# Kernel optimization log

Measured on AMD Instinct MI355X. Metric: run time of the kernel, lower is better.

The kernel has to match this reference:

```python
import jax, jax.numpy as jnp
import numpy as np

B, D_IN, D_HID, D_OUT = 16384, 512, 512, 512
E, K = 8, 2
VQ_COEFF, LB_COEFF = 0.05, 0.01
LOG100 = float(np.log(100.0))
LOG2 = float(np.log(2.0))


def _normalize(v):
    # torch F.normalize(dim=1): x / max(||x||, 1e-12)
    n = jnp.linalg.norm(v, axis=-1, keepdims=True)
    return v / jnp.maximum(n, 1e-12)


def _cv_squared(v):
    # torch .var() is unbiased (ddof=1)
    return jnp.var(v, ddof=1) / (jnp.mean(v) ** 2 + 1e-10)


def _rbm_layer(x, rm, W, b, ca, temp):
    # x: [B, d_in], rm: [E, d_in], W: [E, d_out, d_in], b: [E, d_out]
    rm_n = jax.lax.stop_gradient(_normalize(rm))          # .detach() in source
    nx = _normalize(x)
    dists = nx @ rm_n.T                                    # [B, E]
    top_v, top_i = jax.lax.top_k(dists, K)                 # [B, K]
    tv = jax.nn.softmax(top_v, axis=-1)                    # softmax over top-k
    bsz = dists.shape[0]
    attn = jnp.zeros_like(dists).at[jnp.arange(bsz)[:, None], top_i].set(tv)
    # const_attention is frozen (requires_grad=False)
    inp_att = jnp.exp(jnp.minimum(jax.lax.stop_gradient(ca), LOG100))  # [E]
    # dense gather-compute-scatter: expert e output for every token, masked by attn
    eo = jnp.einsum('bi,eoi->beo', x, W) * inp_att[None, :, None] + b[None, :, :]
    out = jnp.einsum('be,beo->bo', jax.lax.stop_gradient(attn), eo)    # att.detach()
    out = out * jnp.exp(jnp.minimum(temp, LOG100))
    # aux losses (eval mode: no EMA memory update)
    vq = -(nx[:, None, :] * rm_n[top_i]).sum(-1)           # [B, K]
    vq_loss = (tv * vq).sum(-1).mean()
    lb = _cv_squared(attn.sum(0))
    aux = VQ_COEFF * vq_loss + LB_COEFF * lb               # sim_coeff = 0
    return out, aux


def setup_inputs() -> dict:
    key = jax.random.key(0)
    ks = jax.random.split(key, 8)
    x = jax.random.normal(ks[0], (B, D_IN), dtype=jnp.float32)
    rm0 = _normalize(jax.random.normal(ks[1], (E, D_IN), dtype=jnp.float32))
    W0 = jax.random.normal(ks[2], (E, D_HID, D_IN), dtype=jnp.float32) / np.sqrt(D_IN)
    b0 = jnp.zeros((E, D_HID), dtype=jnp.float32)
    rm1 = _normalize(jax.random.normal(ks[3], (E, D_HID), dtype=jnp.float32))
    W1 = jax.random.normal(ks[4], (E, D_OUT, D_HID), dtype=jnp.float32) / np.sqrt(D_HID)
    b1 = jnp.zeros((E, D_OUT), dtype=jnp.float32)
    temp0 = jnp.full((1,), LOG2, dtype=jnp.float32)
    temp1 = jnp.full((1,), LOG2, dtype=jnp.float32)
    ca0 = jnp.zeros((E,), dtype=jnp.float32)
    ca1 = jnp.zeros((E,), dtype=jnp.float32)
    return {"x": x, "rm0": rm0, "W0": W0, "b0": b0, "temp0": temp0, "ca0": ca0,
            "rm1": rm1, "W1": W1, "b1": b1, "temp1": temp1, "ca1": ca1}


def reference(x, rm0, W0, b0, temp0, ca0, rm1, W1, b1, temp1, ca1):
    h0, a0 = _rbm_layer(x, rm0, W0, b0, ca0, temp0)
    h_emb = h0                      # embedding tapped after layer 0 (pre-activation)
    h = jax.nn.relu(h0)             # norm_type=None -> no norm
    h1, a1 = _rbm_layer(h, rm1, W1, b1, ca1, temp1)
    return (h_emb, h1, a0 + a1)
```

## Files before the change

### kernel.cpp

```cpp
#include <hip/hip_runtime.h>
#include <cmath>
#include <cstdint>

#define NTOK   16384
#define NEXP   8
#define DM     512
#define LOG100 4.605170185988092f

typedef _Float16 half8  __attribute__((ext_vector_type(8)));
typedef float    floatx4 __attribute__((ext_vector_type(4)));

#define MFMA_F16(a, b, c) __builtin_amdgcn_mfma_f32_16x16x32_f16((a), (b), (c), 0, 0, 0)

__device__ __forceinline__ void gl_lds16(const void* g, void* l) {
    __builtin_amdgcn_global_load_lds(
        (const __attribute__((address_space(1))) void*)g,
        (__attribute__((address_space(3))) void*)l, 16, 0, 0);
}


__global__ __launch_bounds__(256) void prep_kernel(
    const float* __restrict__ rm0, const float* __restrict__ rm1,
    const float* __restrict__ ca0, const float* __restrict__ ca1,
    const float* __restrict__ temp0, const float* __restrict__ temp1,
    float* __restrict__ ctrl, float* __restrict__ rmn)
{
    int tid = threadIdx.x, lane = tid & 63, w = tid >> 6;
    if (tid < 32) ((int*)ctrl)[tid] = 0;
    if (tid >= 32 && tid < 48) ctrl[tid] = 0.f;
    if (tid == 48 || tid == 49) ctrl[tid] = 0.f;
    if (tid == 50) ctrl[50] = expf(fminf(temp0[0], LOG100));
    if (tid == 51) ctrl[51] = expf(fminf(temp1[0], LOG100));
    if (tid >= 52 && tid < 68) {
        int i = tid - 52;
        ctrl[tid] = expf(fminf(i < 8 ? ca0[i] : ca1[i - 8], LOG100));
    }
    for (int r = w; r < 16; r += 4) {
        const float* src = (r < 8) ? (rm0 + r * DM) : (rm1 + (r - 8) * DM);
        float v[8]; float ss = 0.f;
        #pragma unroll
        for (int j = 0; j < 8; ++j) { v[j] = src[lane + 64 * j]; ss += v[j] * v[j]; }
        #pragma unroll
        for (int off = 32; off > 0; off >>= 1) ss += __shfl_xor(ss, off);
        float inv = 1.f / fmaxf(sqrtf(ss), 1e-12f);
        float* dst = rmn + r * DM;
        #pragma unroll
        for (int j = 0; j < 8; ++j) dst[lane + 64 * j] = v[j] * inv;
    }
}

__global__ __launch_bounds__(256) void pack_w_kernel(
    const float* __restrict__ W0, const float* __restrict__ W1,
    half8* __restrict__ w0pk, half8* __restrict__ w1pk)
{
    int i = blockIdx.x * 256 + threadIdx.x;
    if (i < 512 * 1024) {
        int l = i & 63, j = (i >> 6) & 15, kb = (i >> 10) & 15, nt = (i >> 14) & 3, e = i >> 16;
        int s = l >> 3, p = l & 7, c = p ^ s;
        int n = nt * 128 + j * 8 + s;
        int k = kb * 32 + (c & 3) * 8;
        const float* src = W0 + ((size_t)e * DM + n) * DM + k;
        half8 v;
        #pragma unroll
        for (int t = 0; t < 8; ++t) {
            float f = src[t];
            _Float16 h = (_Float16)f;
            v[t] = (c < 4) ? h : (_Float16)(f - (float)h);
        }
        w0pk[i] = v;
    } else {
        int m = i - 512 * 1024;
        int l = m & 63, j = (m >> 6) & 15, kb = (m >> 10) & 7, nt = (m >> 13) & 3, e = m >> 15;
        int s = l >> 3, p = l & 7, c = p ^ s;
        int n = nt * 128 + j * 8 + s;
        int k = kb * 64 + c * 8;
        const float* src = W1 + ((size_t)e * DM + n) * DM + k;
        half8 v;
        #pragma unroll
        for (int t = 0; t < 8; ++t) v[t] = (_Float16)src[t];
        w1pk[m] = v;
    }
}

__global__ __launch_bounds__(256) void route_kernel(
    const float* __restrict__ src,
    const float* __restrict__ rmn,
    int relu_in, int split,
    _Float16* __restrict__ dst,
    unsigned char* __restrict__ key,
    float2* __restrict__ wts,
    float2* __restrict__ bs)
{
    __shared__ float rmLds[NEXP * DM];
    int tid = threadIdx.x;
    for (int i = tid; i < NEXP * DM; i += 256) rmLds[i] = rmn[i];
    __syncthreads();
    int lane = tid & 63, w = tid >> 6;
    int token = blockIdx.x * 4 + w;

    const float* row = src + (size_t)token * DM;
    float x[8]; float ss = 0.f;
    #pragma unroll
    for (int j = 0; j < 8; ++j) {
        float v = row[lane + 64 * j];
        if (relu_in) v = fmaxf(v, 0.f);
        x[j] = v; ss += v * v;
    }
    if (split) {
        #pragma unroll
        for (int j = 0; j < 8; ++j) {
            int k = lane + 64 * j;
            size_t base = (size_t)token * 1024 + (size_t)((k >> 5) << 6) + (k & 31);
            _Float16 h = (_Float16)x[j];
            dst[base] = h;
            dst[base + 32] = (_Float16)(x[j] - (float)h);
        }
    } else {
        #pragma unroll
        for (int j = 0; j < 8; ++j)
            dst[(size_t)token * DM + lane + 64 * j] = (_Float16)x[j];
    }
    float d[8];
    #pragma unroll
    for (int e = 0; e < 8; ++e) {
        float a = 0.f;
        #pragma unroll
        for (int j = 0; j < 8; ++j) a += x[j] * rmLds[e * DM + lane + 64 * j];
        d[e] = a;
    }
    #pragma unroll
    for (int off = 32; off > 0; off >>= 1) {
        ss += __shfl_xor(ss, off);
        #pragma unroll
        for (int e = 0; e < 8; ++e) d[e] += __shfl_xor(d[e], off);
    }
    float inv = 1.f / fmaxf(sqrtf(ss), 1e-12f);
    float best = -1e30f, second = -1e30f; int be = 0, se = 0;
    #pragma unroll
    for (int e = 0; e < 8; ++e) {
        float de = d[e] * inv;
        if (de > best)        { second = best; se = be; best = de; be = e; }
        else if (de > second) { second = de; se = e; }
    }
    float z = expf(second - best);
    float w0 = 1.f / (1.f + z), w1 = z / (1.f + z);
    if (lane == 0) {
        key[token] = (unsigned char)be;
        key[NTOK + token] = (unsigned char)se;
        wts[token] = make_float2(w0, w1);
        bs[token] = make_float2(best, second);
    }
}

__global__ __launch_bounds__(256) void compact_kernel(
    const unsigned char* __restrict__ key,
    const float2* __restrict__ wts,
    const float2* __restrict__ bs,
    int* __restrict__ cnt,
    unsigned short* __restrict__ bkt,
    float* __restrict__ imp,
    float* __restrict__ vq_acc)
{
    int slot = blockIdx.x >> 3, e = blockIdx.x & 7;
    int chunk = blockIdx.y;
    const unsigned char* k = key + slot * NTOK;
    unsigned short* ob = bkt + (size_t)(slot * 8 + e) * NTOK;
    int tid = threadIdx.x, lane = tid & 63, w = tid >> 6;
    float wsum = 0.f, vqs = 0.f;
    for (int c = 0; c < 8; ++c) {
        int tok = chunk * 2048 + c * 256 + tid;
        bool m = (k[tok] == (unsigned char)e);
        unsigned long long mask = __ballot(m);
        int wcount = __popcll(mask);
        int wbase = 0;
        if (lane == 0 && wcount) wbase = atomicAdd(&cnt[slot * 8 + e], wcount);
        wbase = __shfl(wbase, 0);
        if (m) {
            int pre = __popcll(mask & ((1ull << lane) - 1ull));
            ob[wbase + pre] = (unsigned short)tok;
            float2 wp = wts[tok]; float2 b2 = bs[tok];
            float wv = slot ? wp.y : wp.x;
            wsum += wv;
            vqs  += wv * (slot ? b2.y : b2.x);
        }
    }
    #pragma unroll
    for (int off = 32; off > 0; off >>= 1) {
        wsum += __shfl_xor(wsum, off);
        vqs  += __shfl_xor(vqs, off);
    }
    __shared__ float rw[4], rv[4];
    if (lane == 0) { rw[w] = wsum; rv[w] = vqs; }
    __syncthreads();
    if (tid == 0) {
        atomicAdd(&imp[e], rw[0] + rw[1] + rw[2] + rw[3]);
        atomicAdd(vq_acc, -(rv[0] + rv[1] + rv[2] + rv[3]));
    }
}

template <bool SPLIT>
__global__ __launch_bounds__(256, 3) void gemm_kernel(
    const _Float16* __restrict__ A,
    const _Float16* __restrict__ Wpk,
    const float* __restrict__ bias,
    const float* __restrict__ iav,
    const float* __restrict__ tscp,
    const int* __restrict__ cnt,
    const unsigned short* __restrict__ bkt,
    const float2* __restrict__ wts,
    int slot, int accum,
    float* __restrict__ outp)
{
    __shared__ __align__(16) _Float16 ldsB[2 * 8192];
    __shared__ int tokLds[128];

    int p = blockIdx.x;
    int xcd = p & 7, s = p >> 3;
    int t = xcd * 17 + (s >> 2), nt = s & 3;
    int e = -1, m0 = 0, M = 0, acc0 = 0;
    #pragma unroll
    for (int ee = 0; ee < 8; ++ee) {
        int Me = cnt[ee];
        int ne = (Me + 127) >> 7;
        if (t >= acc0 && t < acc0 + ne) { e = ee; m0 = (t - acc0) << 7; M = Me; }
        acc0 += ne;
    }
    if (e < 0) return;
    int n0 = nt << 7;
    int valid = min(128, M - m0);
    int tid = threadIdx.x, lane = tid & 63, w = tid >> 6;
    if (tid < 128) tokLds[tid] = bkt[e * NTOK + m0 + min(tid, valid - 1)];
    __syncthreads();

    int wm = w >> 1, wn = w & 1;
    int r0 = wm * 64, c0 = wn * 64;
    int q = lane >> 4, l15 = lane & 15;

    constexpr int KIT = SPLIT ? 16 : 8;
    constexpr int AS  = SPLIT ? 1024 : 512;

    const _Float16* Ab[4];
    #pragma unroll
    for (int mi = 0; mi < 4; ++mi)
        Ab[mi] = A + (size_t)tokLds[r0 + mi * 16 + l15] * AS + q * 8;

    const _Float16* wtile = Wpk + (size_t)(e * 4 + nt) * KIT * 8192;

    floatx4 accu[4][4];
    #pragma unroll
    for (int mi = 0; mi < 4; ++mi)
        #pragma unroll
        for (int ni = 0; ni < 4; ++ni) accu[mi][ni] = (floatx4){0.f, 0.f, 0.f, 0.f};

    #pragma unroll
    for (int jj = 0; jj < 4; ++jj) {
        int j = w + jj * 4;
        gl_lds16(wtile + j * 512 + lane * 8, (void*)(ldsB + j * 512));
    }

    #pragma unroll
    for (int kb = 0; kb < KIT; ++kb) {
        half8 ah[4], al[4];
        #pragma unroll
        for (int mi = 0; mi < 4; ++mi) {
            ah[mi] = *(const half8*)(Ab[mi] + kb * 64);
            al[mi] = *(const half8*)(Ab[mi] + kb * 64 + 32);
        }
        if (kb + 1 < KIT) {
            _Float16* dB = ldsB + ((kb + 1) & 1) * 8192;
            const _Float16* wb = wtile + (size_t)(kb + 1) * 8192;
            #pragma unroll
            for (int jj = 0; jj < 4; ++jj) {
                int j = w + jj * 4;
                gl_lds16(wb + j * 512 + lane * 8, (void*)(dB + j * 512));
            }
        }
        if (kb + 1 < KIT) asm volatile("s_waitcnt vmcnt(12)" ::: "memory");
        else              asm volatile("s_waitcnt vmcnt(8)"  ::: "memory");
        __builtin_amdgcn_sched_barrier(0);
        __builtin_amdgcn_s_barrier();
        {
            const _Float16* bB = ldsB + (kb & 1) * 8192;
            #pragma unroll
            for (int ni = 0; ni < 4; ++ni) {
                int r = c0 + ni * 16 + l15;
                int ph = q ^ (r & 7), pl = (q + 4) ^ (r & 7);
                half8 bh = *(const half8*)(bB + r * 64 + ph * 8);
                half8 bl = *(const half8*)(bB + r * 64 + pl * 8);
                if constexpr (SPLIT) {
                    #pragma unroll
                    for (int mi = 0; mi < 4; ++mi) accu[mi][ni] = MFMA_F16(ah[mi], bh, accu[mi][ni]);
                    #pragma unroll
                    for (int mi = 0; mi < 4; ++mi) accu[mi][ni] = MFMA_F16(ah[mi], bl, accu[mi][ni]);
                    #pragma unroll
                    for (int mi = 0; mi < 4; ++mi) accu[mi][ni] = MFMA_F16(al[mi], bh, accu[mi][ni]);
                } else {
                    #pragma unroll
                    for (int mi = 0; mi < 4; ++mi) accu[mi][ni] = MFMA_F16(ah[mi], bh, accu[mi][ni]);
                    #pragma unroll
                    for (int mi = 0; mi < 4; ++mi) accu[mi][ni] = MFMA_F16(al[mi], bl, accu[mi][ni]);
                }
            }
        }
        if (kb + 1 < KIT) {
            __builtin_amdgcn_sched_barrier(0);
            __builtin_amdgcn_s_barrier();
        }
    }

    float tsc = *tscp, iae = iav[e];
    float bv[4];
    #pragma unroll
    for (int ni = 0; ni < 4; ++ni) bv[ni] = bias[e * DM + n0 + c0 + ni * 16 + l15];
    #pragma unroll
    for (int mi = 0; mi < 4; ++mi) {
        int liBase = r0 + mi * 16 + q * 4;
        #pragma unroll
        for (int reg = 0; reg < 4; ++reg) {
            int li = liBase + reg;
            if (li < valid) {
                int tok = tokLds[li];
                float2 wp = wts[tok];
                float wgt = slot ? wp.y : wp.x;
                float sg = tsc * wgt * iae, sb = tsc * wgt;
                float* orow = outp + (size_t)tok * DM + n0;
                #pragma unroll
                for (int ni = 0; ni < 4; ++ni) {
                    float v = accu[mi][ni][reg] * sg + bv[ni] * sb;
                    int c = c0 + ni * 16 + l15;
                    if (accum) orow[c] += v; else orow[c] = v;
                }
            }
        }
    }
}

__global__ void finalize_kernel(const float* __restrict__ ctrl, float* __restrict__ outp)
{
    if (threadIdx.x == 0) {
        float aux = 0.f;
        for (int l = 0; l < 2; ++l) {
            float vq = ctrl[48 + l] / (float)NTOK;
            float mean = 0.f;
            for (int e = 0; e < 8; ++e) mean += ctrl[32 + l * 8 + e];
            mean *= 0.125f;
            float s = 0.f;
            for (int e = 0; e < 8; ++e) {
                float d = ctrl[32 + l * 8 + e] - mean;
                s += d * d;
            }
            float var = s / 7.f;
            float lb = var / (mean * mean + 1e-10f);
            aux += 0.05f * vq + 0.01f * lb;
        }
        *outp = aux;
    }
}

extern "C" void kernel_launch(void* const* d_in, const int* in_sizes, int n_in,
                              void* d_out, int out_size, void* d_ws, size_t ws_size,
                              hipStream_t stream) {
    const float* x     = (const float*)d_in[0];
    const float* rm0   = (const float*)d_in[1];
    const float* W0    = (const float*)d_in[2];
    const float* b0    = (const float*)d_in[3];
    const float* temp0 = (const float*)d_in[4];
    const float* ca0   = (const float*)d_in[5];
    const float* rm1   = (const float*)d_in[6];
    const float* W1    = (const float*)d_in[7];
    const float* b1    = (const float*)d_in[8];
    const float* temp1 = (const float*)d_in[9];
    const float* ca1   = (const float*)d_in[10];
    float* out = (float*)d_out;

    char* ws = (char*)d_ws;
    float* ctrl = (float*)ws;
    int*   cnt  = (int*)ctrl;
    float* imp  = ctrl + 32;
    float* vq   = ctrl + 48;
    float* tsc  = ctrl + 50;
    float* ia   = ctrl + 52;
    float* rmn  = ctrl + 128;
    float2*        wts = (float2*)(ws + (size_t)64  * 1024);
    float2*        bs  = (float2*)(ws + (size_t)384 * 1024);
    unsigned char* key = (unsigned char*)(ws + (size_t)704 * 1024);

    char* big = ws + (1 << 20);
    half8*          w0pk8 = (half8*)(big);
    half8*          w1pk8 = (half8*)(big + (size_t)8  * 1024 * 1024);
    const _Float16* w0pk  = (const _Float16*)w0pk8;
    const _Float16* w1pk  = (const _Float16*)w1pk8;
    _Float16*       h16   = (_Float16*)(big + (size_t)12 * 1024 * 1024);
    unsigned short* bkt   = (unsigned short*)(big + (size_t)28 * 1024 * 1024);

    _Float16* xpk = (_Float16*)(out + (size_t)NTOK * DM);

    prep_kernel<<<1, 256, 0, stream>>>(rm0, rm1, ca0, ca1, temp0, temp1, ctrl, rmn);
    pack_w_kernel<<<3072, 256, 0, stream>>>(W0, W1, w0pk8, w1pk8);

    route_kernel<<<4096, 256, 0, stream>>>(x, rmn, 0, 1, xpk, key, wts, bs);
    compact_kernel<<<dim3(16, 8), 256, 0, stream>>>(key, wts, bs, cnt, bkt, imp, vq);
    gemm_kernel<true><<<544, 256, 0, stream>>>(xpk, w0pk, b0, ia, tsc,
        cnt, bkt, wts, 0, 0, out);
    gemm_kernel<true><<<544, 256, 0, stream>>>(xpk, w0pk, b0, ia, tsc,
        cnt + 8, bkt + 8 * NTOK, wts, 1, 1, out);

    route_kernel<<<4096, 256, 0, stream>>>(out, rmn + 4096, 1, 0, h16,
        key + 2 * NTOK, wts + NTOK, bs + NTOK);
    compact_kernel<<<dim3(16, 8), 256, 0, stream>>>(key + 2 * NTOK, wts + NTOK, bs + NTOK,
        cnt + 16, bkt + 16 * NTOK, imp + 8, vq + 1);
    gemm_kernel<false><<<544, 256, 0, stream>>>(h16, w1pk, b1, ia + 8, tsc + 1,
        cnt + 16, bkt + 16 * NTOK, wts + NTOK, 0, 0, out + (size_t)NTOK * DM);
    gemm_kernel<false><<<544, 256, 0, stream>>>(h16, w1pk, b1, ia + 8, tsc + 1,
        cnt + 24, bkt + 24 * NTOK, wts + NTOK, 1, 1, out + (size_t)NTOK * DM);

    finalize_kernel<<<1, 64, 0, stream>>>(ctrl, out + (size_t)2 * NTOK * DM);
}
```

Baseline: 485.3 us.

## Merge top-k slot GEMMs into one atomic-accumulating launch and fold prep into pack

The two per-slot expert GEMM launches in each layer become one launch over 16 buckets (slot × expert). Both slots now add into the output with fp32 global atomic adds, and the route kernel zeroes each output row beforehand. The separate prep kernel is folded into an extra block of the weight-pack kernel, and GEMM launch bounds rise to 4 waves per SIMD. The aim is fewer launches, less serialization between slot passes and better tail fill, at the cost of atomic traffic, extra zero-store bandwidth, nondeterministic summation order and possible register pressure.

```diff
diff --git a/kernel.cpp b/kernel.cpp
--- a/kernel.cpp
+++ b/kernel.cpp
@@ -18,41 +18,48 @@
         (__attribute__((address_space(3))) void*)l, 16, 0, 0);
 }
 
-
-__global__ __launch_bounds__(256) void prep_kernel(
+__device__ __forceinline__ void atomAddF(float* p, float v) {
+#if __has_builtin(__builtin_amdgcn_global_atomic_fadd_f32)
+    __builtin_amdgcn_global_atomic_fadd_f32((__attribute__((address_space(1))) float*)p, v);
+#else
+    atomicAdd(p, v);
+#endif
+}
+
+
+__global__ __launch_bounds__(256) void pack_w_kernel(
+    const float* __restrict__ W0, const float* __restrict__ W1,
+    half8* __restrict__ w0pk, half8* __restrict__ w1pk,
     const float* __restrict__ rm0, const float* __restrict__ rm1,
     const float* __restrict__ ca0, const float* __restrict__ ca1,
     const float* __restrict__ temp0, const float* __restrict__ temp1,
     float* __restrict__ ctrl, float* __restrict__ rmn)
 {
-    int tid = threadIdx.x, lane = tid & 63, w = tid >> 6;
-    if (tid < 32) ((int*)ctrl)[tid] = 0;
-    if (tid >= 32 && tid < 48) ctrl[tid] = 0.f;
-    if (tid == 48 || tid == 49) ctrl[tid] = 0.f;
-    if (tid == 50) ctrl[50] = expf(fminf(temp0[0], LOG100));
-    if (tid == 51) ctrl[51] = expf(fminf(temp1[0], LOG100));
-    if (tid >= 52 && tid < 68) {
-        int i = tid - 52;
-        ctrl[tid] = expf(fminf(i < 8 ? ca0[i] : ca1[i - 8], LOG100));
-    }
-    for (int r = w; r < 16; r += 4) {
-        const float* src = (r < 8) ? (rm0 + r * DM) : (rm1 + (r - 8) * DM);
-        float v[8]; float ss = 0.f;
-        #pragma unroll
-        for (int j = 0; j < 8; ++j) { v[j] = src[lane + 64 * j]; ss += v[j] * v[j]; }
-        #pragma unroll
-        for (int off = 32; off > 0; off >>= 1) ss += __shfl_xor(ss, off);
-        float inv = 1.f / fmaxf(sqrtf(ss), 1e-12f);
-        float* dst = rmn + r * DM;
-        #pragma unroll
-        for (int j = 0; j < 8; ++j) dst[lane + 64 * j] = v[j] * inv;
-    }
-}
-
-__global__ __launch_bounds__(256) void pack_w_kernel(
-    const float* __restrict__ W0, const float* __restrict__ W1,
-    half8* __restrict__ w0pk, half8* __restrict__ w1pk)
-{
+    if (blockIdx.x == 3072) {
+        int tid = threadIdx.x, lane = tid & 63, w = tid >> 6;
+        if (tid < 32) ((int*)ctrl)[tid] = 0;
+        if (tid >= 32 && tid < 48) ctrl[tid] = 0.f;
+        if (tid == 48 || tid == 49) ctrl[tid] = 0.f;
+        if (tid == 50) ctrl[50] = expf(fminf(temp0[0], LOG100));
+        if (tid == 51) ctrl[51] = expf(fminf(temp1[0], LOG100));
+        if (tid >= 52 && tid < 68) {
+            int i = tid - 52;
+            ctrl[tid] = expf(fminf(i < 8 ? ca0[i] : ca1[i - 8], LOG100));
+        }
+        for (int r = w; r < 16; r += 4) {
+            const float* src = (r < 8) ? (rm0 + r * DM) : (rm1 + (r - 8) * DM);
+            float v[8]; float ss = 0.f;
+            #pragma unroll
+            for (int j = 0; j < 8; ++j) { v[j] = src[lane + 64 * j]; ss += v[j] * v[j]; }
+            #pragma unroll
+            for (int off = 32; off > 0; off >>= 1) ss += __shfl_xor(ss, off);
+            float inv = 1.f / fmaxf(sqrtf(ss), 1e-12f);
+            float* dst = rmn + r * DM;
+            #pragma unroll
+            for (int j = 0; j < 8; ++j) dst[lane + 64 * j] = v[j] * inv;
+        }
+        return;
+    }
     int i = blockIdx.x * 256 + threadIdx.x;
     if (i < 512 * 1024) {
         int l = i & 63, j = (i >> 6) & 15, kb = (i >> 10) & 15, nt = (i >> 14) & 3, e = i >> 16;
@@ -89,7 +96,8 @@
     _Float16* __restrict__ dst,
     unsigned char* __restrict__ key,
     float2* __restrict__ wts,
-    float2* __restrict__ bs)
+    float2* __restrict__ bs,
+    float* __restrict__ zrow)
 {
     __shared__ float rmLds[NEXP * DM];
     int tid = threadIdx.x;
@@ -97,6 +105,13 @@
     __syncthreads();
     int lane = tid & 63, w = tid >> 6;
     int token = blockIdx.x * 4 + w;
+
+    {
+        float4 z4 = {0.f, 0.f, 0.f, 0.f};
+        float4* zp = (float4*)(zrow + (size_t)token * DM);
+        zp[lane] = z4;
+        zp[lane + 64] = z4;
+    }
 
     const float* row = src + (size_t)token * DM;
     float x[8]; float ss = 0.f;
@@ -199,16 +214,15 @@
 }
 
 template <bool SPLIT>
-__global__ __launch_bounds__(256, 3) void gemm_kernel(
+__global__ __launch_bounds__(256, 4) void gemm_kernel(
     const _Float16* __restrict__ A,
     const _Float16* __restrict__ Wpk,
     const float* __restrict__ bias,
     const float* __restrict__ iav,
     const float* __restrict__ tscp,
-    const int* __restrict__ cnt,
+    const int* __restrict__ cnt16,
     const unsigned short* __restrict__ bkt,
     const float2* __restrict__ wts,
-    int slot, int accum,
     float* __restrict__ outp)
 {
     __shared__ __align__(16) _Float16 ldsB[2 * 8192];
@@ -216,20 +230,21 @@
 
     int p = blockIdx.x;
     int xcd = p & 7, s = p >> 3;
-    int t = xcd * 17 + (s >> 2), nt = s & 3;
-    int e = -1, m0 = 0, M = 0, acc0 = 0;
-    #pragma unroll
-    for (int ee = 0; ee < 8; ++ee) {
-        int Me = cnt[ee];
+    int t = xcd * 34 + (s >> 2), nt = s & 3;
+    int b = -1, m0 = 0, M = 0, acc0 = 0;
+    #pragma unroll
+    for (int bb = 0; bb < 16; ++bb) {
+        int Me = cnt16[bb];
         int ne = (Me + 127) >> 7;
-        if (t >= acc0 && t < acc0 + ne) { e = ee; m0 = (t - acc0) << 7; M = Me; }
+        if (t >= acc0 && t < acc0 + ne) { b = bb; m0 = (t - acc0) << 7; M = Me; }
         acc0 += ne;
     }
-    if (e < 0) return;
+    if (b < 0) return;
+    int slot = b >> 3, e = b & 7;
     int n0 = nt << 7;
     int valid = min(128, M - m0);
     int tid = threadIdx.x, lane = tid & 63, w = tid >> 6;
-    if (tid < 128) tokLds[tid] = bkt[e * NTOK + m0 + min(tid, valid - 1)];
+    if (tid < 128) tokLds[tid] = bkt[(size_t)b * NTOK + m0 + min(tid, valid - 1)];
     __syncthreads();
 
     int wm = w >> 1, wn = w & 1;
@@ -328,7 +343,7 @@
                 for (int ni = 0; ni < 4; ++ni) {
                     float v = accu[mi][ni][reg] * sg + bv[ni] * sb;
                     int c = c0 + ni * 16 + l15;
-                    if (accum) orow[c] += v; else orow[c] = v;
+                    atomAddF(&orow[c], v);
                 }
             }
         }
@@ -395,24 +410,20 @@
 
     _Float16* xpk = (_Float16*)(out + (size_t)NTOK * DM);
 
-    prep_kernel<<<1, 256, 0, stream>>>(rm0, rm1, ca0, ca1, temp0, temp1, ctrl, rmn);
-    pack_w_kernel<<<3072, 256, 0, stream>>>(W0, W1, w0pk8, w1pk8);
-
-    route_kernel<<<4096, 256, 0, stream>>>(x, rmn, 0, 1, xpk, key, wts, bs);
+    pack_w_kernel<<<3073, 256, 0, stream>>>(W0, W1, w0pk8, w1pk8,
+        rm0, rm1, ca0, ca1, temp0, temp1, ctrl, rmn);
+
+    route_kernel<<<4096, 256, 0, stream>>>(x, rmn, 0, 1, xpk, key, wts, bs, out);
     compact_kernel<<<dim3(16, 8), 256, 0, stream>>>(key, wts, bs, cnt, bkt, imp, vq);
-    gemm_kernel<true><<<544, 256, 0, stream>>>(xpk, w0pk, b0, ia, tsc,
-        cnt, bkt, wts, 0, 0, out);
-    gemm_kernel<true><<<544, 256, 0, stream>>>(xpk, w0pk, b0, ia, tsc,
-        cnt + 8, bkt + 8 * NTOK, wts, 1, 1, out);
+    gemm_kernel<true><<<1088, 256, 0, stream>>>(xpk, w0pk, b0, ia, tsc,
+        cnt, bkt, wts, out);
 
     route_kernel<<<4096, 256, 0, stream>>>(out, rmn + 4096, 1, 0, h16,
-        key + 2 * NTOK, wts + NTOK, bs + NTOK);
+        key + 2 * NTOK, wts + NTOK, bs + NTOK, out + (size_t)NTOK * DM);
     compact_kernel<<<dim3(16, 8), 256, 0, stream>>>(key + 2 * NTOK, wts + NTOK, bs + NTOK,
         cnt + 16, bkt + 16 * NTOK, imp + 8, vq + 1);
-    gemm_kernel<false><<<544, 256, 0, stream>>>(h16, w1pk, b1, ia + 8, tsc + 1,
-        cnt + 16, bkt + 16 * NTOK, wts + NTOK, 0, 0, out + (size_t)NTOK * DM);
-    gemm_kernel<false><<<544, 256, 0, stream>>>(h16, w1pk, b1, ia + 8, tsc + 1,
-        cnt + 24, bkt + 24 * NTOK, wts + NTOK, 1, 1, out + (size_t)NTOK * DM);
+    gemm_kernel<false><<<1088, 256, 0, stream>>>(h16, w1pk, b1, ia + 8, tsc + 1,
+        cnt + 16, bkt + 16 * NTOK, wts + NTOK, out + (size_t)NTOK * DM);
 
     finalize_kernel<<<1, 64, 0, stream>>>(ctrl, out + (size_t)2 * NTOK * DM);
 }
```

After: 460.6 us. -5.1%, faster.
